# Performance work log

Hardware: AMD Instinct MI355X
Metric: run time of the kernel (lower is better)

The kernel has to match this reference:

```python
import jax, jax.numpy as jnp
import numpy as np

CHUNK = 32      # args.chunk_size
MEM = 64        # args.mem_size (fixed-capacity steady state)
EPS = 1e-10


def setup_inputs() -> dict:
    key = jax.random.key(0)
    k1, k2 = jax.random.split(key)
    x = jax.random.normal(k1, (16, 4096, 512), dtype=jnp.float32)
    mem_init = jax.random.normal(k2, (16, 64, 512), dtype=jnp.float32)
    return {"x": x, "mem_init": mem_init}


def _memory_bank_update(x, mem_init):
    B, T, D = x.shape
    C, M = CHUNK, MEM
    n_chunks = T // C
    xc = x[:, : n_chunks * C].reshape(B, n_chunks, C, D).transpose(1, 0, 2, 3)  # [n,B,C,D]
    inv_sqrt_d = 1.0 / jnp.sqrt(jnp.asarray(D, x.dtype))
    # threshold = 0.5 * log2(mem_size) as in the source
    threshold = 0.5 * jnp.log2(jnp.asarray(M, x.dtype) + EPS)

    def step(carry, chunk):  # chunk: [B, C, D]
        mem, m_score, m_freq = carry
        # cross-attention score of chunk tokens over memory slots
        logits = jnp.einsum('bcd,bmd->bcm', chunk, mem) * inv_sqrt_d
        score = jax.nn.softmax(logits, axis=-1).mean(axis=1)          # [B, M]
        new_m = chunk.max(axis=1)                                      # maxpool over chunk -> [B, D]
        entropy = (-jnp.log2(score + EPS) * score).sum(axis=1).mean()  # scalar (mean over batch)

        # --- path 1 (entropy > threshold): score-based slot replacement ---
        ms1 = m_score + score
        mf1 = m_freq + 1.0
        repl = jnp.argmin(ms1 / mf1, axis=1)                           # lowest avg-score slot, [B]
        oh1 = jax.nn.one_hot(repl, M, dtype=mem.dtype)                 # [B, M]
        mem1 = mem * (1.0 - oh1[..., None]) + oh1[..., None] * new_m[:, None, :]
        ms1 = ms1 * (1.0 - oh1)          # fresh slot starts with zero score
        mf1 = mf1 * (1.0 - oh1) + oh1    # and freq 1

        # --- path 2 (entropy <= threshold): cosine-sim nearest-slot merge ---
        nmn = new_m / jnp.sqrt((new_m * new_m).sum(-1, keepdims=True) + 1e-8)
        mn = mem / jnp.sqrt((mem * mem).sum(-1, keepdims=True) + 1e-8)
        sim = jnp.einsum('bd,bmd->bm', nmn, mn)                        # [B, M]
        idx = jnp.argmax(sim, axis=1)
        oh2 = jax.nn.one_hot(idx, M, dtype=mem.dtype)
        # mem[b,idx] += 0.7*new_m - 0.7*mem[b,idx]  ->  0.3*old + 0.7*new
        mem2 = mem + oh2[..., None] * (0.7 * new_m[:, None, :] - 0.7 * mem)

        take1 = entropy > threshold
        mem_n = jnp.where(take1, mem1, mem2)
        ms_n = jnp.where(take1, ms1, m_score)
        mf_n = jnp.where(take1, mf1, m_freq)
        return (mem_n, ms_n, mf_n), score

    init = (mem_init,
            jnp.zeros((B, M), x.dtype),
            jnp.zeros((B, M), x.dtype))
    (mem, m_score, m_freq), _ = jax.lax.scan(step, init, xc)
    return mem  # [B, M, D]


def reference(x, mem_init):
    return _memory_bank_update(x, mem_init)
```

## Files before the change

kernel.cpp:

```cpp
#include <hip/hip_runtime.h>
#include <stdint.h>

#define NB 16
#define TT 4096
#define DD 512
#define CC 32
#define MM 64
#define NCH 128
#define NSRC 192
#define ROWW 36
#define TOTROWS 16320
#define KS 32

#define WS_NEWM 0
#define WS_NN2  (NB*NCH*DD)
#define WS_GX   (WS_NN2 + NB*NCH)
#define WS_CTL  (WS_GX + (size_t)NB*TOTROWS*ROWW)
#define WS_TOTAL_BYTES (WS_CTL*4 + (size_t)NB*16*8)

__device__ __forceinline__ float wredsum(float v){
#pragma unroll
  for (int o = 32; o > 0; o >>= 1) v += __shfl_xor(v, o);
  return v;
}
__device__ __forceinline__ float wredmax(float v){
#pragma unroll
  for (int o = 32; o > 0; o >>= 1) v = fmaxf(v, __shfl_xor(v, o));
  return v;
}

__global__ __launch_bounds__(256)
void k1_newm(const float* __restrict__ x, float* __restrict__ ws)
{
  __shared__ float part[4];
  const int bid = blockIdx.x;
  const int b = bid >> 7, t = bid & 127;
  const int tid = threadIdx.x;
  const float* xb = x + ((size_t)b*TT + (size_t)t*CC)*DD;
  const int k0 = tid*2;
  float v0 = -INFINITY, v1 = -INFINITY;
#pragma unroll
  for (int c = 0; c < CC; ++c){
    const float2 xv = *(const float2*)(xb + (size_t)c*DD + k0);
    v0 = fmaxf(v0, xv.x); v1 = fmaxf(v1, xv.y);
  }
  float* nm = ws + WS_NEWM + ((size_t)b*NCH + t)*DD;
  nm[k0] = v0; nm[k0+1] = v1;
  float p = wredsum(v0*v0 + v1*v1);
  if ((tid & 63) == 0) part[tid >> 6] = p;
  __syncthreads();
  if (tid == 0) ws[WS_NN2 + (size_t)b*NCH + t] = part[0]+part[1]+part[2]+part[3];
}

__global__ __launch_bounds__(512)
void k2_gemm(const float* __restrict__ x, const float* __restrict__ mem_init,
             float* __restrict__ ws)
{
  __shared__ float Xs[KS][128];
  __shared__ float Ss[KS][NSRC];

  const int b  = blockIdx.x;
  const int tg = blockIdx.y;
  const int tid = threadIdx.x;
  const int rowlim = min(NSRC, 68 + 4*tg);
  const int T0 = tg*128;

  const int ot = tid & 15;
  const int rs = tid >> 4;
  const bool active = (rs*6 < rowlim);

  float acc[6][8];
#pragma unroll
  for (int j = 0; j < 6; ++j)
#pragma unroll
    for (int i = 0; i < 8; ++i) acc[j][i] = 0.0f;

  const float* xb    = x + ((size_t)b*TT + T0)*DD;
  const float* nmarr = ws + WS_NEWM + (size_t)b*NCH*DD;

  const int xtok = tid >> 2;
  const int xkq  = tid & 3;
  const int srow = tid >> 1;
  const int shalf= tid & 1;
  const float* srcrow = nullptr;
  if (tid < 384 && srow < rowlim)
    srcrow = (srow < MM) ? (mem_init + ((size_t)b*MM + srow)*DD)
                         : (nmarr + (size_t)(srow - MM)*DD);

  for (int ks = 0; ks < DD/KS; ++ks){
    const int k0 = ks*KS;
    {
      const float* p = xb + (size_t)xtok*DD + k0 + xkq*8;
      const float4 a  = *(const float4*)p;
      const float4 c4 = *(const float4*)(p + 4);
      const int kb = xkq*8;
      Xs[kb+0][xtok]=a.x;  Xs[kb+1][xtok]=a.y;  Xs[kb+2][xtok]=a.z;  Xs[kb+3][xtok]=a.w;
      Xs[kb+4][xtok]=c4.x; Xs[kb+5][xtok]=c4.y; Xs[kb+6][xtok]=c4.z; Xs[kb+7][xtok]=c4.w;
    }
    if (srcrow){
      const float* p = srcrow + k0 + shalf*16;
#pragma unroll
      for (int q = 0; q < 4; ++q){
        const float4 a = *(const float4*)(p + q*4);
        const int kb = shalf*16 + q*4;
        Ss[kb+0][srow]=a.x; Ss[kb+1][srow]=a.y; Ss[kb+2][srow]=a.z; Ss[kb+3][srow]=a.w;
      }
    }
    __syncthreads();
    if (active){
#pragma unroll
      for (int k = 0; k < KS; ++k){
        const float4 x0 = *(const float4*)&Xs[k][ot*8];
        const float4 x1 = *(const float4*)&Xs[k][ot*8 + 4];
        const float2 r0 = *(const float2*)&Ss[k][rs*6];
        const float2 r1 = *(const float2*)&Ss[k][rs*6 + 2];
        const float2 r2 = *(const float2*)&Ss[k][rs*6 + 4];
        const float xv[8] = {x0.x,x0.y,x0.z,x0.w,x1.x,x1.y,x1.z,x1.w};
        const float rv[6] = {r0.x,r0.y,r1.x,r1.y,r2.x,r2.y};
#pragma unroll
        for (int j = 0; j < 6; ++j)
#pragma unroll
          for (int i = 0; i < 8; ++i)
            acc[j][i] = fmaf(rv[j], xv[i], acc[j][i]);
      }
    }
    __syncthreads();
  }

  const float inv_sqrt_d = 1.0f / sqrtf((float)DD);
  const int t  = tg*4 + (ot >> 2);
  const int c0 = (ot & 3)*8;
  float* gbase = ws + WS_GX + ((size_t)b*TOTROWS + (size_t)(64*t + (t*(t-1))/2))*ROWW;
#pragma unroll
  for (int j = 0; j < 6; ++j){
    const int row = rs*6 + j;
    if (row < 64 + t){
      float* g = gbase + (size_t)row*ROWW + c0;
      float4 o0 = {acc[j][0]*inv_sqrt_d, acc[j][1]*inv_sqrt_d,
                   acc[j][2]*inv_sqrt_d, acc[j][3]*inv_sqrt_d};
      float4 o1 = {acc[j][4]*inv_sqrt_d, acc[j][5]*inv_sqrt_d,
                   acc[j][6]*inv_sqrt_d, acc[j][7]*inv_sqrt_d};
      *(float4*)g = o0;
      *(float4*)(g + 4) = o1;
    }
  }
}

__global__ __launch_bounds__(256)
void k2_nn(const float* __restrict__ mem_init, float* __restrict__ ws)
{
  __shared__ float nm[DD];
  const int b = blockIdx.x, t = blockIdx.y;
  const int tid = threadIdx.x, lane = tid & 63, w = tid >> 6;
  const float* nmarr = ws + WS_NEWM + (size_t)b*NCH*DD;
  {
    const float2 v = *(const float2*)(nmarr + (size_t)t*DD + tid*2);
    nm[tid*2] = v.x; nm[tid*2+1] = v.y;
  }
  __syncthreads();
  const float4 na = *(const float4*)(nm + lane*8);
  const float4 nc = *(const float4*)(nm + lane*8 + 4);
  const int nrows = MM + t;
  float* gbase = ws + WS_GX + ((size_t)b*TOTROWS + (size_t)(64*t + (t*(t-1))/2))*ROWW;
  for (int r = w; r < nrows; r += 4){
    const float* src = (r < MM) ? (mem_init + ((size_t)b*MM + r)*DD)
                                : (nmarr + (size_t)(r - MM)*DD);
    const float4 a  = *(const float4*)(src + lane*8);
    const float4 c4 = *(const float4*)(src + lane*8 + 4);
    float d = a.x*na.x + a.y*na.y + a.z*na.z + a.w*na.w
            + c4.x*nc.x + c4.y*nc.y + c4.z*nc.z + c4.w*nc.w;
    d = wredsum(d);
    if (lane == 0) gbase[(size_t)r*ROWW + 32] = d;
  }
}

__global__ __launch_bounds__(1024)
void k3_scan(const float* __restrict__ mem_init, float* __restrict__ ws,
             float* __restrict__ out)
{
  __shared__ float red0[CC*65];
  __shared__ float dense[MM][NSRC];
  __shared__ float s_spart[16][MM];
  __shared__ float s_score[MM], s_sc[MM], s_fr[MM], s_n2[MM], s_simdot[MM];
  __shared__ int   s_srcRow[MM], s_isC[MM];
  __shared__ float s_entvals[NB];
  __shared__ int   s_take1, s_idx1, s_idx2, s_chg;

  const int tid  = threadIdx.x;
  const int lane = tid & 63;
  const int w    = tid >> 6;
  const int b    = blockIdx.x;
  const int wu   = __builtin_amdgcn_readfirstlane(w);

  const float* newmarr = ws + WS_NEWM;
  const float* nn2arr  = ws + WS_NN2;
  const float* gx      = ws + WS_GX;
  unsigned long long* ctl = (unsigned long long*)(ws + WS_CTL);

  if (tid < MM){ s_sc[tid] = 0.0f; s_fr[tid] = 0.0f; s_srcRow[tid] = tid; s_isC[tid] = 0; }
  if (tid == 0) s_chg = -1;
#pragma unroll
  for (int it = 0; it < 4; ++it){
    const int m0 = wu + it*16;
    const float* src = mem_init + ((size_t)b*MM + m0)*DD;
    const float4 a  = *(const float4*)(src + lane*8);
    const float4 c4 = *(const float4*)(src + lane*8 + 4);
    float p = a.x*a.x + a.y*a.y + a.z*a.z + a.w*a.w
            + c4.x*c4.x + c4.y*c4.y + c4.z*c4.z + c4.w*c4.w;
    p = wredsum(p);
    if (lane == 0) s_n2[m0] = p;
  }
  __syncthreads();

  const int  m   = tid >> 4;
  const int  c2  = (tid & 15)*2;
  const bool sdl = ((tid & 15) == 0);
  float pv0 = 0.0f, pv1 = 0.0f, psd = 0.0f;

  for (int t = 0; t < NCH; ++t){
    const float nn2_t = nn2arr[(size_t)b*NCH + t];
    const float* gxb = gx + ((size_t)b*TOTROWS + (size_t)(64*t + (t*(t-1))/2))*ROWW;

    {
      float v0, v1;
      if (!s_isC[m]){
        if (t == 0 || m == s_chg){
          const float* grow = gxb + (size_t)s_srcRow[m]*ROWW;
          const float2 p = *(const float2*)(grow + c2);
          v0 = p.x; v1 = p.y;
          if (sdl) s_simdot[m] = grow[32];
        } else {
          v0 = pv0; v1 = pv1;
          if (sdl) s_simdot[m] = psd;
        }
      } else {
        v0 = 0.0f; v1 = 0.0f; float sd = 0.0f;
        const int ns = 64 + t;
        for (int s = 0; s < ns; ++s){
          const float co = dense[m][s];
          if (co != 0.0f){
            const float* grow = gxb + (size_t)s*ROWW;
            v0 = fmaf(co, grow[c2],   v0);
            v1 = fmaf(co, grow[c2+1], v1);
            if (sdl) sd = fmaf(co, grow[32], sd);
          }
        }
        if (sdl) s_simdot[m] = sd;
      }
      red0[c2*65 + m]     = v0;
      red0[(c2+1)*65 + m] = v1;
    }
    __syncthreads();

    {
      const float a0 = red0[(2*w)*65 + lane];
      const float a1 = red0[(2*w+1)*65 + lane];
      const float mx0 = wredmax(a0), mx1 = wredmax(a1);
      const float e0 = expf(a0 - mx0), e1 = expf(a1 - mx1);
      const float su0 = wredsum(e0), su1 = wredsum(e1);
      s_spart[w][lane] = e0/su0 + e1/su1;
    }
    __syncthreads();

    if (t+1 < NCH && !s_isC[m]){
      const float* growN = gx + ((size_t)b*TOTROWS + (size_t)(64*(t+1) + ((t+1)*t)/2))*ROWW
                              + (size_t)s_srcRow[m]*ROWW;
      const float2 p = *(const float2*)(growN + c2);
      pv0 = p.x; pv1 = p.y;
      if (sdl) psd = growN[32];
    }

    if (wu == 0){
      float s = 0.0f;
#pragma unroll
      for (int i = 0; i < 16; ++i) s += s_spart[i][lane];
      s *= (1.0f/32.0f);
      s_score[lane] = s;
      const float ent = wredsum(-log2f(s + 1e-10f) * s);
      if (lane == 0){
        const unsigned long long v =
            ((unsigned long long)(unsigned)(t+1) << 32) |
            (unsigned long long)__float_as_uint(ent);
        __hip_atomic_store(&ctl[b*16 + (t&1)], v, __ATOMIC_RELEASE, __HIP_MEMORY_SCOPE_AGENT);
      }
      {
        float q = (s_sc[lane] + s) / (s_fr[lane] + 1.0f);
        int idx = lane;
#pragma unroll
        for (int o = 32; o > 0; o >>= 1){
          const float ov = __shfl_xor(q, o);
          const int   oi = __shfl_xor(idx, o);
          if (ov < q || (ov == q && oi < idx)){ q = ov; idx = oi; }
        }
        if (lane == 0) s_idx1 = idx;
      }
      if (lane < NB){
        unsigned long long vv;
        do {
          vv = __hip_atomic_load(&ctl[lane*16 + (t&1)], __ATOMIC_ACQUIRE, __HIP_MEMORY_SCOPE_AGENT);
        } while ((unsigned)(vv >> 32) != (unsigned)(t+1));
        s_entvals[lane] = __uint_as_float((unsigned)vv);
      }
      if (lane == 0){
        float es = 0.0f;
        for (int i = 0; i < NB; ++i) es += s_entvals[i];
        s_take1 = ((es * (1.0f/16.0f)) > 3.0f) ? 1 : 0;
      }
    } else if (wu == 1){
      float sim = s_simdot[lane] / (sqrtf(nn2_t + 1e-8f) * sqrtf(s_n2[lane] + 1e-8f));
      int idx = lane;
#pragma unroll
      for (int o = 32; o > 0; o >>= 1){
        const float ov = __shfl_xor(sim, o);
        const int   oi = __shfl_xor(idx, o);
        if (ov > sim || (ov == sim && oi < idx)){ sim = ov; idx = oi; }
      }
      if (lane == 0) s_idx2 = idx;
    }
    __syncthreads();

    if (s_take1){
      if (tid < MM){
        float ns = s_sc[tid] + s_score[tid];
        float nf = s_fr[tid] + 1.0f;
        if (tid == s_idx1){ ns = 0.0f; nf = 1.0f; }
        s_sc[tid] = ns; s_fr[tid] = nf;
      }
      if (tid == 512){
        const int rr = s_idx1;
        s_isC[rr] = 0; s_srcRow[rr] = 64 + t; s_n2[rr] = nn2_t; s_chg = rr;
      }
    } else {
      const int i = s_idx2;
      const int oldC = s_isC[i];
      const int oldR = s_srcRow[i];
      __syncthreads();
      if (tid < NSRC){
        float val = oldC ? 0.3f*dense[i][tid] : ((tid == oldR) ? 0.3f : 0.0f);
        if (tid == 64 + t) val += 0.7f;
        dense[i][tid] = val;
      }
      if (tid == 512){
        s_isC[i] = 1;
        s_n2[i] = 0.09f*s_n2[i] + 0.42f*s_simdot[i] + 0.49f*nn2_t;
        s_chg = i;
      }
    }
    __syncthreads();
  }

#pragma unroll
  for (int it = 0; it < 4; ++it){
    const int mo = wu + it*16;
    const int k0 = lane*8;
    float o8[8];
    if (!s_isC[mo]){
      const int row = s_srcRow[mo];
      const float* vec = (row < MM) ? (mem_init + ((size_t)b*MM + row)*DD)
                                    : (newmarr + ((size_t)b*NCH + (row - MM))*DD);
#pragma unroll
      for (int j = 0; j < 8; ++j) o8[j] = vec[k0 + j];
    } else {
#pragma unroll
      for (int j = 0; j < 8; ++j) o8[j] = 0.0f;
      for (int s = 0; s < NSRC; ++s){
        const float co = dense[mo][s];
        if (co != 0.0f){
          const float* vec = (s < MM) ? (mem_init + ((size_t)b*MM + s)*DD)
                                      : (newmarr + ((size_t)b*NCH + (s - MM))*DD);
#pragma unroll
          for (int j = 0; j < 8; ++j) o8[j] = fmaf(co, vec[k0 + j], o8[j]);
        }
      }
    }
    float* dst = out + ((size_t)b*MM + mo)*DD + k0;
#pragma unroll
    for (int j = 0; j < 8; ++j) dst[j] = o8[j];
  }
}

extern "C" void kernel_launch(void* const* d_in, const int* in_sizes, int n_in,
                              void* d_out, int out_size, void* d_ws, size_t ws_size,
                              hipStream_t stream)
{
  const float* x  = (const float*)d_in[0];
  const float* mi = (const float*)d_in[1];
  float* out = (float*)d_out;
  float* ws  = (float*)d_ws;
  hipLaunchKernelGGL(k1_newm, dim3(NB*NCH), dim3(256), 0, stream, x, ws);
  hipLaunchKernelGGL(k2_gemm, dim3(NB, 32), dim3(512), 0, stream, x, mi, ws);
  hipLaunchKernelGGL(k2_nn,   dim3(NB, NCH), dim3(256), 0, stream, mi, ws);
  hipLaunchKernelGGL(k3_scan, dim3(NB), dim3(1024), 0, stream, mi, ws, out);
}
```

Measured before the change: 839.0 us.

## Speculate both branch outcomes to overlap cross-batch entropy sync with next-step logits

The sequential scan kernel now computes next-chunk logits and both candidate score vectors (replacement and merge paths) before the cross-block entropy decision is known. It does this by incrementally patching a cached softmax base (subtracting one slot's exponent and adding the new one). The grid-wide entropy handshake for step t is thus waited on only after the speculative work for step t+1 is done, which takes the global spin-wait off the critical path. In exchange it adds extra LDS buffers and duplicated score and entropy computation per step. It also reuses the old row max when patching, which may differ numerically from a full softmax.

```diff
diff --git a/kernel.cpp b/kernel.cpp
--- a/kernel.cpp
+++ b/kernel.cpp
@@ -16,7 +16,6 @@
 #define WS_NN2  (NB*NCH*DD)
 #define WS_GX   (WS_NN2 + NB*NCH)
 #define WS_CTL  (WS_GX + (size_t)NB*TOTROWS*ROWW)
-#define WS_TOTAL_BYTES (WS_CTL*4 + (size_t)NB*16*8)
 
 __device__ __forceinline__ float wredsum(float v){
 #pragma unroll
@@ -178,13 +177,19 @@
 void k3_scan(const float* __restrict__ mem_init, float* __restrict__ ws,
              float* __restrict__ out)
 {
-  __shared__ float red0[CC*65];
+  __shared__ float Llds[CC][65];
+  __shared__ float Elds[CC][65];
+  __shared__ float P1[16][65];
+  __shared__ float P2[16][65];
   __shared__ float dense[MM][NSRC];
-  __shared__ float s_spart[16][MM];
-  __shared__ float s_score[MM], s_sc[MM], s_fr[MM], s_n2[MM], s_simdot[MM];
+  __shared__ float S_base[CC], Mx[CC], E1c[CC], E2c[CC], R1[CC], R2[CC];
+  __shared__ float s_sc[MM], s_fr[MM], s_n2[MM];
+  __shared__ float s_sdB[MM];
+  __shared__ float s_sdCur[MM];
+  __shared__ float s_scoreP[MM], s_scoreC[MM];
   __shared__ int   s_srcRow[MM], s_isC[MM];
-  __shared__ float s_entvals[NB];
-  __shared__ int   s_take1, s_idx1, s_idx2, s_chg;
+  __shared__ float s_rnmNN, s_sd1v, s_sd2v, s_n2v1, s_n2v2;
+  __shared__ int   s_d, s_i1p, s_i2p, s_oldC2, s_oldR2;
 
   const int tid  = threadIdx.x;
   const int lane = tid & 63;
@@ -197,8 +202,11 @@
   const float* gx      = ws + WS_GX;
   unsigned long long* ctl = (unsigned long long*)(ws + WS_CTL);
 
-  if (tid < MM){ s_sc[tid] = 0.0f; s_fr[tid] = 0.0f; s_srcRow[tid] = tid; s_isC[tid] = 0; }
-  if (tid == 0) s_chg = -1;
+  const int  gm  = tid >> 4;
+  const int  gc2 = (tid & 15)*2;
+  const bool gl  = ((tid & 15) == 0);
+
+  if (tid < MM){ s_sc[tid]=0.f; s_fr[tid]=0.f; s_srcRow[tid]=tid; s_isC[tid]=0; }
 #pragma unroll
   for (int it = 0; it < 4; ++it){
     const int m0 = wu + it*16;
@@ -212,102 +220,137 @@
   }
   __syncthreads();
 
-  const int  m   = tid >> 4;
-  const int  c2  = (tid & 15)*2;
-  const bool sdl = ((tid & 15) == 0);
-  float pv0 = 0.0f, pv1 = 0.0f, psd = 0.0f;
+  {
+    const float* gx0 = gx + (size_t)b*TOTROWS*ROWW;
+    const float* grow = gx0 + (size_t)gm*ROWW;
+    const float2 p = *(const float2*)(grow + gc2);
+    Llds[gc2][gm] = p.x; Llds[gc2+1][gm] = p.y;
+    if (gl) s_sdCur[gm] = grow[32];
+  }
+  __syncthreads();
+  {
+#pragma unroll
+    for (int rr = 0; rr < 2; ++rr){
+      const int c = 2*wu + rr;
+      const float l = Llds[c][lane];
+      const float mx = wredmax(l);
+      const float e = expf(l - mx);
+      const float S = wredsum(e);
+      Elds[c][lane] = e;
+      if (lane == 0){ S_base[c] = S; Mx[c] = mx; }
+    }
+  }
+  __syncthreads();
+  {
+    const int m = tid & 63, g = tid >> 6;
+    const int c0 = 2*g, c1 = c0 + 1;
+    P1[g][m] = Elds[c0][m]/S_base[c0] + Elds[c1][m]/S_base[c1];
+  }
+  __syncthreads();
+  if (wu == 0){
+    float s0 = 0.f;
+#pragma unroll
+    for (int g = 0; g < 16; ++g) s0 += P1[g][lane];
+    s0 *= 0.03125f;
+    s_scoreC[lane] = s0;
+    const float ent0 = wredsum(-log2f(s0 + 1e-10f) * s0);
+    if (lane == 0){
+      const unsigned long long v = ((unsigned long long)1u << 32)
+                                 | (unsigned long long)__float_as_uint(ent0);
+      __hip_atomic_store(&ctl[b], v, __ATOMIC_RELEASE, __HIP_MEMORY_SCOPE_AGENT);
+    }
+  }
+  __syncthreads();
 
   for (int t = 0; t < NCH; ++t){
     const float nn2_t = nn2arr[(size_t)b*NCH + t];
-    const float* gxb = gx + ((size_t)b*TOTROWS + (size_t)(64*t + (t*(t-1))/2))*ROWW;
-
-    {
-      float v0, v1;
-      if (!s_isC[m]){
-        if (t == 0 || m == s_chg){
-          const float* grow = gxb + (size_t)s_srcRow[m]*ROWW;
-          const float2 p = *(const float2*)(grow + c2);
-          v0 = p.x; v1 = p.y;
-          if (sdl) s_simdot[m] = grow[32];
-        } else {
-          v0 = pv0; v1 = pv1;
-          if (sdl) s_simdot[m] = psd;
+
+    if (t > 0){
+      const int d = s_d;
+      const int m1 = s_i1p, m2 = s_i2p;
+      if (d){
+        if (tid < MM){
+          float ns = s_sc[tid] + s_scoreP[tid];
+          float nf = s_fr[tid] + 1.0f;
+          if (tid == m1){ ns = 0.0f; nf = 1.0f; }
+          s_sc[tid] = ns; s_fr[tid] = nf;
+          s_sdCur[tid] = (tid == m1) ? s_sd1v : s_sdB[tid];
+        }
+        if (tid == 512){
+          s_srcRow[m1] = 64 + (t-1);
+          s_isC[m1] = 0;
+          s_n2[m1] = s_n2v1;
         }
       } else {
-        v0 = 0.0f; v1 = 0.0f; float sd = 0.0f;
-        const int ns = 64 + t;
-        for (int s = 0; s < ns; ++s){
-          const float co = dense[m][s];
+        if (tid < NSRC){
+          float val = s_oldC2 ? 0.3f*dense[m2][tid] : ((tid == s_oldR2) ? 0.3f : 0.0f);
+          if (tid == 64 + (t-1)) val += 0.7f;
+          dense[m2][tid] = val;
+        }
+        if (tid < MM) s_sdCur[tid] = (tid == m2) ? s_sd2v : s_sdB[tid];
+        if (tid == 512){
+          s_isC[m2] = 1;
+          s_n2[m2] = s_n2v2;
+        }
+      }
+    }
+    __syncthreads();
+
+    if (t < NCH-1){
+      const float* gxn = gx + ((size_t)b*TOTROWS
+                         + (size_t)(64*(t+1) + ((t+1)*t)/2))*ROWW;
+      float v0, v1, sd = 0.f;
+      if (!s_isC[gm]){
+        const float* grow = gxn + (size_t)s_srcRow[gm]*ROWW;
+        const float2 p = *(const float2*)(grow + gc2);
+        v0 = p.x; v1 = p.y;
+        if (gl) sd = grow[32];
+      } else {
+        v0 = 0.f; v1 = 0.f;
+        const int ns = 65 + t;
+        for (int s2 = 0; s2 < ns; ++s2){
+          const float co = dense[gm][s2];
           if (co != 0.0f){
-            const float* grow = gxb + (size_t)s*ROWW;
-            v0 = fmaf(co, grow[c2],   v0);
-            v1 = fmaf(co, grow[c2+1], v1);
-            if (sdl) sd = fmaf(co, grow[32], sd);
+            const float* grow = gxn + (size_t)s2*ROWW;
+            v0 = fmaf(co, grow[gc2],   v0);
+            v1 = fmaf(co, grow[gc2+1], v1);
+            if (gl) sd = fmaf(co, grow[32], sd);
           }
         }
-        if (sdl) s_simdot[m] = sd;
-      }
-      red0[c2*65 + m]     = v0;
-      red0[(c2+1)*65 + m] = v1;
-    }
-    __syncthreads();
-
-    {
-      const float a0 = red0[(2*w)*65 + lane];
-      const float a1 = red0[(2*w+1)*65 + lane];
-      const float mx0 = wredmax(a0), mx1 = wredmax(a1);
-      const float e0 = expf(a0 - mx0), e1 = expf(a1 - mx1);
-      const float su0 = wredsum(e0), su1 = wredsum(e1);
-      s_spart[w][lane] = e0/su0 + e1/su1;
-    }
-    __syncthreads();
-
-    if (t+1 < NCH && !s_isC[m]){
-      const float* growN = gx + ((size_t)b*TOTROWS + (size_t)(64*(t+1) + ((t+1)*t)/2))*ROWW
-                              + (size_t)s_srcRow[m]*ROWW;
-      const float2 p = *(const float2*)(growN + c2);
-      pv0 = p.x; pv1 = p.y;
-      if (sdl) psd = growN[32];
-    }
+      }
+      Llds[gc2][gm] = v0; Llds[gc2+1][gm] = v1;
+      if (gl) s_sdB[gm] = sd;
+      if (tid < 32) {
+        Llds[tid][64] = gxn[(size_t)(64+t)*ROWW + tid];
+      }
+      if (tid == 32) s_rnmNN = gxn[(size_t)(64+t)*ROWW + 32];
+    }
+    __syncthreads();
 
     if (wu == 0){
-      float s = 0.0f;
-#pragma unroll
-      for (int i = 0; i < 16; ++i) s += s_spart[i][lane];
-      s *= (1.0f/32.0f);
-      s_score[lane] = s;
-      const float ent = wredsum(-log2f(s + 1e-10f) * s);
-      if (lane == 0){
-        const unsigned long long v =
-            ((unsigned long long)(unsigned)(t+1) << 32) |
-            (unsigned long long)__float_as_uint(ent);
-        __hip_atomic_store(&ctl[b*16 + (t&1)], v, __ATOMIC_RELEASE, __HIP_MEMORY_SCOPE_AGENT);
-      }
-      {
-        float q = (s_sc[lane] + s) / (s_fr[lane] + 1.0f);
-        int idx = lane;
-#pragma unroll
-        for (int o = 32; o > 0; o >>= 1){
-          const float ov = __shfl_xor(q, o);
-          const int   oi = __shfl_xor(idx, o);
-          if (ov < q || (ov == q && oi < idx)){ q = ov; idx = oi; }
-        }
-        if (lane == 0) s_idx1 = idx;
-      }
-      if (lane < NB){
-        unsigned long long vv;
-        do {
-          vv = __hip_atomic_load(&ctl[lane*16 + (t&1)], __ATOMIC_ACQUIRE, __HIP_MEMORY_SCOPE_AGENT);
-        } while ((unsigned)(vv >> 32) != (unsigned)(t+1));
-        s_entvals[lane] = __uint_as_float((unsigned)vv);
-      }
-      if (lane == 0){
-        float es = 0.0f;
-        for (int i = 0; i < NB; ++i) es += s_entvals[i];
-        s_take1 = ((es * (1.0f/16.0f)) > 3.0f) ? 1 : 0;
+      float q = (s_sc[lane] + s_scoreC[lane]) / (s_fr[lane] + 1.0f);
+      int idx = lane;
+#pragma unroll
+      for (int o = 32; o > 0; o >>= 1){
+        const float ov = __shfl_xor(q, o);
+        const int   oi = __shfl_xor(idx, o);
+        if (ov < q || (ov == q && oi < idx)){ q = ov; idx = oi; }
+      }
+      if (lane == 0) s_i1p = idx;
+      if (t < NCH-1){
+#pragma unroll
+        for (int rr = 0; rr < 2; ++rr){
+          const int c = 28 + rr;
+          const float l = Llds[c][lane];
+          const float mx = wredmax(l);
+          const float e = expf(l - mx);
+          const float S = wredsum(e);
+          Elds[c][lane] = e;
+          if (lane == 0){ S_base[c] = S; Mx[c] = mx; }
+        }
       }
     } else if (wu == 1){
-      float sim = s_simdot[lane] / (sqrtf(nn2_t + 1e-8f) * sqrtf(s_n2[lane] + 1e-8f));
+      float sim = s_sdCur[lane] / (sqrtf(nn2_t + 1e-8f) * sqrtf(s_n2[lane] + 1e-8f));
       int idx = lane;
 #pragma unroll
       for (int o = 32; o > 0; o >>= 1){
@@ -315,39 +358,124 @@
         const int   oi = __shfl_xor(idx, o);
         if (ov > sim || (ov == sim && oi < idx)){ sim = ov; idx = oi; }
       }
-      if (lane == 0) s_idx2 = idx;
-    }
-    __syncthreads();
-
-    if (s_take1){
-      if (tid < MM){
-        float ns = s_sc[tid] + s_score[tid];
-        float nf = s_fr[tid] + 1.0f;
-        if (tid == s_idx1){ ns = 0.0f; nf = 1.0f; }
-        s_sc[tid] = ns; s_fr[tid] = nf;
-      }
-      if (tid == 512){
-        const int rr = s_idx1;
-        s_isC[rr] = 0; s_srcRow[rr] = 64 + t; s_n2[rr] = nn2_t; s_chg = rr;
+      if (lane == 0){
+        s_i2p = idx;
+        s_oldC2 = s_isC[idx];
+        s_oldR2 = s_srcRow[idx];
+        s_n2v2 = 0.09f*s_n2[idx] + 0.42f*s_sdCur[idx] + 0.49f*nn2_t;
+        s_n2v1 = nn2_t;
+      }
+      if (t < NCH-1){
+#pragma unroll
+        for (int rr = 0; rr < 2; ++rr){
+          const int c = 30 + rr;
+          const float l = Llds[c][lane];
+          const float mx = wredmax(l);
+          const float e = expf(l - mx);
+          const float S = wredsum(e);
+          Elds[c][lane] = e;
+          if (lane == 0){ S_base[c] = S; Mx[c] = mx; }
+        }
       }
     } else {
-      const int i = s_idx2;
-      const int oldC = s_isC[i];
-      const int oldR = s_srcRow[i];
-      __syncthreads();
+      if (t < NCH-1){
+#pragma unroll
+        for (int rr = 0; rr < 2; ++rr){
+          const int c = 2*(wu-2) + rr;
+          const float l = Llds[c][lane];
+          const float mx = wredmax(l);
+          const float e = expf(l - mx);
+          const float S = wredsum(e);
+          Elds[c][lane] = e;
+          if (lane == 0){ S_base[c] = S; Mx[c] = mx; }
+        }
+      }
+    }
+    __syncthreads();
+
+    if (t < NCH-1){
+      if (wu == 0 && lane < 32){
+        const int c = lane;
+        const int m1 = s_i1p;
+        const float e1 = expf(Llds[c][64] - Mx[c]);
+        const float S1 = S_base[c] - Elds[c][m1] + e1;
+        E1c[c] = e1; R1[c] = 1.0f / S1;
+        if (c == 0) s_sd1v = s_rnmNN;
+      } else if (wu == 1 && lane < 32){
+        const int c = lane;
+        const int m2 = s_i2p;
+        const float l2 = 0.3f*Llds[c][m2] + 0.7f*Llds[c][64];
+        const float e2 = expf(l2 - Mx[c]);
+        const float S2 = S_base[c] - Elds[c][m2] + e2;
+        E2c[c] = e2; R2[c] = 1.0f / S2;
+        if (c == 0) s_sd2v = 0.3f*s_sdB[m2] + 0.7f*s_rnmNN;
+      }
+    }
+    __syncthreads();
+
+    if (t < NCH-1){
+      const int m = tid & 63, g = tid >> 6;
+      const int c0 = 2*g, c1 = c0 + 1;
+      const int m1 = s_i1p, m2 = s_i2p;
+      const float ea0 = Elds[c0][m], ea1 = Elds[c1][m];
+      const float p1 = ((m==m1)?E1c[c0]:ea0)*R1[c0] + ((m==m1)?E1c[c1]:ea1)*R1[c1];
+      const float p2 = ((m==m2)?E2c[c0]:ea0)*R2[c0] + ((m==m2)?E2c[c1]:ea1)*R2[c1];
+      P1[g][m] = p1;
+      P2[g][m] = p2;
+    }
+    __syncthreads();
+
+    if (wu == 0){
+      float s1 = 0.f, s2 = 0.f, ent1 = 0.f, ent2 = 0.f;
+      if (t < NCH-1){
+#pragma unroll
+        for (int g = 0; g < 16; ++g){ s1 += P1[g][lane]; s2 += P2[g][lane]; }
+        s1 *= 0.03125f; s2 *= 0.03125f;
+        ent1 = wredsum(-log2f(s1 + 1e-10f) * s1);
+        ent2 = wredsum(-log2f(s2 + 1e-10f) * s2);
+      }
+      float ev = 0.f;
+      if (lane < NB){
+        unsigned long long vv;
+        do {
+          vv = __hip_atomic_load(&ctl[(t&1)*16 + lane], __ATOMIC_ACQUIRE,
+                                 __HIP_MEMORY_SCOPE_AGENT);
+        } while ((unsigned)(vv >> 32) != (unsigned)(t+1));
+        ev = __uint_as_float((unsigned)vv);
+      }
+      const float tot = wredsum(ev);
+      const int d = (tot * (1.0f/16.0f) > 3.0f) ? 1 : 0;
+      if (t < NCH-1){
+        if (lane == 0){
+          const float entp = d ? ent1 : ent2;
+          const unsigned long long v = ((unsigned long long)(unsigned)(t+2) << 32)
+                                     | (unsigned long long)__float_as_uint(entp);
+          __hip_atomic_store(&ctl[((t+1)&1)*16 + b], v, __ATOMIC_RELEASE,
+                             __HIP_MEMORY_SCOPE_AGENT);
+        }
+        s_scoreP[lane] = s_scoreC[lane];
+        s_scoreC[lane] = d ? s1 : s2;
+      }
+      if (lane == 0) s_d = d;
+    }
+    __syncthreads();
+  }
+
+  {
+    const int d = s_d;
+    if (d){
+      if (tid == 0){ s_srcRow[s_i1p] = 64 + (NCH-1); s_isC[s_i1p] = 0; }
+    } else {
+      const int i = s_i2p;
       if (tid < NSRC){
-        float val = oldC ? 0.3f*dense[i][tid] : ((tid == oldR) ? 0.3f : 0.0f);
-        if (tid == 64 + t) val += 0.7f;
+        float val = s_oldC2 ? 0.3f*dense[i][tid] : ((tid == s_oldR2) ? 0.3f : 0.0f);
+        if (tid == 64 + (NCH-1)) val += 0.7f;
         dense[i][tid] = val;
       }
-      if (tid == 512){
-        s_isC[i] = 1;
-        s_n2[i] = 0.09f*s_n2[i] + 0.42f*s_simdot[i] + 0.49f*nn2_t;
-        s_chg = i;
-      }
-    }
-    __syncthreads();
-  }
+      if (tid == 0) s_isC[i] = 1;
+    }
+  }
+  __syncthreads();
 
 #pragma unroll
   for (int it = 0; it < 4; ++it){
```

Result: slower. 943.5 us (+12.5%).
